# Kernel tuning notes

Hardware: AMD Instinct MI355X
Metric: run time of the kernel (lower is better)

The kernel has to match this reference:

```python
import jax, jax.numpy as jnp
import numpy as np

N_CUST = 500000
N_FUND = 50000
N_EDGE = 4000000
D_CUST = 101
D_FUND = 1
HID = 64


def setup_inputs() -> dict:
    key = jax.random.key(0)
    ks = jax.random.split(key, 16)
    s = lambda fan_in: 1.0 / np.sqrt(fan_in)
    return {
        "x_customer": jax.random.normal(ks[0], (N_CUST, D_CUST), jnp.float32),
        "x_fund": jax.random.normal(ks[1], (N_FUND, D_FUND), jnp.float32),
        "src_fund": jax.random.randint(ks[2], (N_EDGE,), 0, N_FUND, jnp.int64),
        "dst_customer": jax.random.randint(ks[3], (N_EDGE,), 0, N_CUST, jnp.int64),
        # per-node-type input projections
        "W_cust": jax.random.uniform(ks[4], (D_CUST, HID), jnp.float32, -s(D_CUST), s(D_CUST)),
        "b_cust": jax.random.uniform(ks[5], (HID,), jnp.float32, -s(D_CUST), s(D_CUST)),
        "W_fund": jax.random.uniform(ks[6], (D_FUND, HID), jnp.float32, -s(D_FUND), s(D_FUND)),
        "b_fund": jax.random.uniform(ks[7], (HID,), jnp.float32, -s(D_FUND), s(D_FUND)),
        # SAGEConv fund->customer: lin_l (neighbor aggr, bias) + lin_r (self, no bias)
        "W_l": jax.random.uniform(ks[8], (HID, HID), jnp.float32, -s(HID), s(HID)),
        "b_l": jax.random.uniform(ks[9], (HID,), jnp.float32, -s(HID), s(HID)),
        "W_r": jax.random.uniform(ks[10], (HID, HID), jnp.float32, -s(HID), s(HID)),
        # output head
        "W_out": jax.random.uniform(ks[11], (HID, 2), jnp.float32, -s(HID), s(HID)),
        "b_out": jax.random.uniform(ks[12], (2,), jnp.float32, -s(HID), s(HID)),
    }


def reference(x_customer, x_fund, src_fund, dst_customer,
              W_cust, b_cust, W_fund, b_fund, W_l, b_l, W_r, W_out, b_out):
    # per-node-type linear + relu
    h_c = jax.nn.relu(x_customer @ W_cust + b_cust)  # [N_CUST, HID]
    h_f = jax.nn.relu(x_fund @ W_fund + b_fund)      # [N_FUND, HID]

    # SAGEConv (fund -> customer): gather src fund features per edge,
    # mean-aggregate by destination customer (scatter-sum / count)
    msgs = h_f[src_fund]  # [N_EDGE, HID]
    summed = jax.ops.segment_sum(msgs, dst_customer, num_segments=N_CUST)
    cnt = jax.ops.segment_sum(jnp.ones((msgs.shape[0],), msgs.dtype),
                              dst_customer, num_segments=N_CUST)
    mean = summed / jnp.maximum(cnt, 1.0)[:, None]

    out_c = mean @ W_l + b_l + h_c @ W_r  # SAGE: lin_l(aggr) + lin_r(self)
    return out_c @ W_out + b_out          # [N_CUST, 2]
```

## Files before the change

kernel.cpp:

```cpp
#include <hip/hip_runtime.h>
#include <stdint.h>

#define N_CUST 500000
#define N_FUND 50000
#define N_EDGE 4000000
#define D_CUST 101
#define HID 64

#define NB   512
#define EPB  ((N_EDGE + NB - 1) / NB)
#define CB   512
#define NBKT ((N_CUST + CB - 1) / CB)
#define CAP  8192
#define TPB  32

typedef float  float4u __attribute__((ext_vector_type(4), aligned(4)));
using frag_ab = __attribute__((ext_vector_type(8))) short;
using frag_cd = __attribute__((ext_vector_type(4))) float;

struct __align__(16) Accum { float g0, g1, cnt, pad; };

__device__ __forceinline__ short f2bf(float f) {
    unsigned u = __float_as_uint(f);
    u += 0x7fffu + ((u >> 16) & 1u);
    return (short)(u >> 16);
}

__global__ __launch_bounds__(256) void k_gf(
    const float* __restrict__ x_fund,
    const float* __restrict__ W_fund,
    const float* __restrict__ b_fund,
    const float* __restrict__ W_l,
    const float* __restrict__ W_out,
    float2* __restrict__ gf)
{
    __shared__ float sAf[128];
    __shared__ float sWf[64];
    __shared__ float sBf[64];
    int t = threadIdx.x;
    if (t < 128) {
        int h = t >> 1, j = t & 1;
        float s = 0.f;
        for (int k = 0; k < 64; ++k)
            s = fmaf(W_l[h * 64 + k], W_out[k * 2 + j], s);
        sAf[t] = s;
    } else if (t < 192) {
        sWf[t - 128] = W_fund[t - 128];
    } else {
        sBf[t - 192] = b_fund[t - 192];
    }
    __syncthreads();

    int f = blockIdx.x * 256 + t;
    if (f >= N_FUND) return;
    float xf = x_fund[f];
    float g0 = 0.f, g1 = 0.f;
    #pragma unroll
    for (int h = 0; h < 64; ++h) {
        float hf = fmaxf(fmaf(xf, sWf[h], sBf[h]), 0.f);
        g0 = fmaf(hf, sAf[2 * h + 0], g0);
        g1 = fmaf(hf, sAf[2 * h + 1], g1);
    }
    gf[f] = make_float2(g0, g1);
}

__global__ __launch_bounds__(256) void k_reorder(
    const int* __restrict__ src, const int* __restrict__ dst,
    unsigned* __restrict__ gcur, unsigned* __restrict__ recs)
{
    __shared__ unsigned hist[NBKT];
    __shared__ unsigned localOff[NBKT];
    __shared__ unsigned cur[NBKT];
    __shared__ unsigned baseG[NBKT];
    __shared__ unsigned ldsRec[EPB];
    __shared__ unsigned short ldsBkt[EPB];

    int t = threadIdx.x, b = blockIdx.x;
    int e0 = b * EPB, e1 = min(e0 + EPB, N_EDGE);
    int cntE = e1 - e0;

    for (int k = t; k < NBKT; k += 256) hist[k] = 0;
    __syncthreads();
    for (int e = e0 + t; e < e1; e += 256)
        atomicAdd(&hist[((unsigned)dst[e]) >> 9], 1u);
    __syncthreads();

    if (t < 64) {
        unsigned v[16], pre[16], run = 0;
        #pragma unroll
        for (int j = 0; j < 16; ++j) {
            int idx = t * 16 + j;
            v[j] = (idx < NBKT) ? hist[idx] : 0u;
            pre[j] = run; run += v[j];
        }
        unsigned sc = run;
        #pragma unroll
        for (int d = 1; d < 64; d <<= 1) {
            unsigned n = __shfl_up(sc, d, 64);
            if (t >= d) sc += n;
        }
        unsigned lane_excl = sc - run;
        #pragma unroll
        for (int j = 0; j < 16; ++j) {
            int idx = t * 16 + j;
            if (idx < NBKT) {
                localOff[idx] = lane_excl + pre[j];
                cur[idx]      = lane_excl + pre[j];
            }
        }
    }
    __syncthreads();

    for (int k = t; k < NBKT; k += 256) {
        unsigned h = hist[k];
        baseG[k] = h ? ((unsigned)k * CAP + atomicAdd(&gcur[k], h)) : 0u;
    }

    for (int e = e0 + t; e < e1; e += 256) {
        unsigned d = (unsigned)dst[e];
        unsigned s = (unsigned)src[e];
        unsigned k = d >> 9;
        unsigned p = atomicAdd(&cur[k], 1u);
        ldsRec[p] = s | ((d & 511u) << 16);
        ldsBkt[p] = (unsigned short)k;
    }
    __syncthreads();

    for (int i = t; i < cntE; i += 256) {
        unsigned k = ldsBkt[i];
        unsigned g = baseG[k] + (i - localOff[k]);
        recs[g] = ldsRec[i];
    }
}

__global__ __launch_bounds__(256) void k_bucket(
    const unsigned* __restrict__ recs, const unsigned* __restrict__ gcur,
    const float2* __restrict__ gf,
    const float* __restrict__ x, const float* __restrict__ Wc,
    const float* __restrict__ bc,
    const float* __restrict__ W_r, const float* __restrict__ W_out,
    const float* __restrict__ b_l, const float* __restrict__ b_out,
    float2* __restrict__ out)
{
    __shared__ float s0[CB], s1[CB], scn[CB];
    __shared__ float sBt[128];
    __shared__ float sc2[2];
    __shared__ float zb[4][16 * 68];

    int t = threadIdx.x, k = blockIdx.x;

    if (t < 128) {
        int h = t >> 1, j = t & 1;
        float s = 0.f;
        for (int kk = 0; kk < 64; ++kk)
            s = fmaf(W_r[h * 64 + kk], W_out[kk * 2 + j], s);
        sBt[t] = s;
    } else if (t < 130) {
        int j = t - 128;
        float s = b_out[j];
        for (int kk = 0; kk < 64; ++kk)
            s = fmaf(b_l[kk], W_out[kk * 2 + j], s);
        sc2[j] = s;
    }
    for (int c = t; c < CB; c += 256) { s0[c] = 0.f; s1[c] = 0.f; scn[c] = 0.f; }
    __syncthreads();

    unsigned r0 = (unsigned)k * CAP, r1 = r0 + gcur[k];
    for (unsigned i = r0 + t; i < r1; i += 256) {
        unsigned r = recs[i];
        float2 g = gf[r & 0xFFFFu];
        unsigned dl = r >> 16;
        atomicAdd(&s0[dl], g.x);
        atomicAdd(&s1[dl], g.y);
        atomicAdd(&scn[dl], 1.f);
    }

    int w = t >> 6, lane = t & 63;
    int c = lane & 15, q = lane >> 4;
    float* z = zb[w];
    frag_ab bfrag[4][4];
    for (int nt = 0; nt < 4; ++nt)
        for (int kc = 0; kc < 4; ++kc) {
            frag_ab f;
            for (int j = 0; j < 8; ++j) {
                int kk = kc * 32 + q * 8 + j;
                int h = nt * 16 + c;
                f[j] = (kk < D_CUST) ? f2bf(Wc[kk * HID + h]) : (short)0;
            }
            bfrag[nt][kc] = f;
        }
    float bcv[4];
    #pragma unroll
    for (int nt = 0; nt < 4; ++nt) bcv[nt] = bc[nt * 16 + c];
    __syncthreads();

    float c20 = sc2[0], c21 = sc2[1];
    int cust0 = k * CB;
    int n_tiles = min(TPB, (N_CUST - cust0) >> 4);

    for (int tl = w; tl < n_tiles; tl += 4) {
        int lrow = tl * 16 + c;
        int row = cust0 + lrow;
        const float* xr = x + (size_t)row * D_CUST;
        frag_ab af[4];
        #pragma unroll
        for (int kc = 0; kc < 3; ++kc) {
            float4u lo = *(const float4u*)(xr + kc * 32 + q * 8);
            float4u hi = *(const float4u*)(xr + kc * 32 + q * 8 + 4);
            frag_ab f;
            f[0]=f2bf(lo[0]); f[1]=f2bf(lo[1]); f[2]=f2bf(lo[2]); f[3]=f2bf(lo[3]);
            f[4]=f2bf(hi[0]); f[5]=f2bf(hi[1]); f[6]=f2bf(hi[2]); f[7]=f2bf(hi[3]);
            af[kc] = f;
        }
        {
            frag_ab f = {0,0,0,0,0,0,0,0};
            if (q == 0) {
                float4u lo = *(const float4u*)(xr + 96);
                f[0]=f2bf(lo[0]); f[1]=f2bf(lo[1]); f[2]=f2bf(lo[2]); f[3]=f2bf(lo[3]);
                f[4]=f2bf(xr[100]);
            }
            af[3] = f;
        }
        frag_cd acc[4];
        #pragma unroll
        for (int nt = 0; nt < 4; ++nt)
            acc[nt] = (frag_cd){bcv[nt], bcv[nt], bcv[nt], bcv[nt]};
        #pragma unroll
        for (int kc = 0; kc < 4; ++kc)
            #pragma unroll
            for (int nt = 0; nt < 4; ++nt)
                acc[nt] = __builtin_amdgcn_mfma_f32_16x16x32_bf16(
                    af[kc], bfrag[nt][kc], acc[nt], 0, 0, 0);

        #pragma unroll
        for (int nt = 0; nt < 4; ++nt)
            #pragma unroll
            for (int i = 0; i < 4; ++i)
                z[(q * 4 + i) * 68 + nt * 16 + c] = fmaxf(acc[nt][i], 0.f);

        float p0 = 0.f, p1 = 0.f;
        #pragma unroll
        for (int j4 = 0; j4 < 4; ++j4) {
            float4u zv = *(const float4u*)(z + c * 68 + q * 16 + j4 * 4);
            float4u b0 = *(const float4u*)(sBt + q * 32 + j4 * 8);
            float4u b1 = *(const float4u*)(sBt + q * 32 + j4 * 8 + 4);
            p0 = fmaf(zv[0], b0[0], p0); p1 = fmaf(zv[0], b0[1], p1);
            p0 = fmaf(zv[1], b0[2], p0); p1 = fmaf(zv[1], b0[3], p1);
            p0 = fmaf(zv[2], b1[0], p0); p1 = fmaf(zv[2], b1[1], p1);
            p0 = fmaf(zv[3], b1[2], p0); p1 = fmaf(zv[3], b1[3], p1);
        }
        p0 += __shfl_xor(p0, 16, 64); p0 += __shfl_xor(p0, 32, 64);
        p1 += __shfl_xor(p1, 16, 64); p1 += __shfl_xor(p1, 32, 64);
        if (q == 0) {
            float inv = 1.0f / fmaxf(scn[lrow], 1.0f);
            out[cust0 + lrow] = make_float2(fmaf(s0[lrow], inv, p0 + c20),
                                            fmaf(s1[lrow], inv, p1 + c21));
        }
    }
}

__global__ __launch_bounds__(256) void k_prep_fb(
    const float* __restrict__ W_r, const float* __restrict__ W_out,
    const float* __restrict__ b_l, const float* __restrict__ b_out,
    float* __restrict__ Bt, float* __restrict__ c2)
{
    int t = threadIdx.x;
    if (t < 128) {
        int h = t >> 1, j = t & 1;
        float s = 0.f;
        for (int k = 0; k < 64; ++k)
            s = fmaf(W_r[h * 64 + k], W_out[k * 2 + j], s);
        Bt[t] = s;
    } else if (t < 130) {
        int j = t - 128;
        float s = b_out[j];
        for (int k = 0; k < 64; ++k)
            s = fmaf(b_l[k], W_out[k * 2 + j], s);
        c2[j] = s;
    }
}

__global__ __launch_bounds__(256) void k_scatter_direct(
    const int* __restrict__ src, const int* __restrict__ dst,
    const float2* __restrict__ gf, Accum* __restrict__ A)
{
    int stride = gridDim.x * 256;
    for (int e = blockIdx.x * 256 + threadIdx.x; e < N_EDGE; e += stride) {
        int s = src[e], d = dst[e];
        float2 g = gf[s];
        unsafeAtomicAdd(&A[d].g0, g.x);
        unsafeAtomicAdd(&A[d].g1, g.y);
        unsafeAtomicAdd(&A[d].cnt, 1.0f);
    }
}

__global__ __launch_bounds__(256) void k_cust_fb(
    const float* __restrict__ x, const float* __restrict__ Wc,
    const float* __restrict__ bc, const float* __restrict__ Bt,
    const float* __restrict__ c2, const Accum* __restrict__ A,
    float2* __restrict__ out)
{
    __shared__ float zb[4][16 * 68];
    __shared__ float sBt[128];
    int tid = threadIdx.x;
    int w = tid >> 6, lane = tid & 63;
    int c = lane & 15, q = lane >> 4;
    float* z = zb[w];
    if (tid < 128) sBt[tid] = Bt[tid];

    frag_ab bfrag[4][4];
    for (int nt = 0; nt < 4; ++nt)
        for (int kc = 0; kc < 4; ++kc) {
            frag_ab f;
            for (int j = 0; j < 8; ++j) {
                int k = kc * 32 + q * 8 + j;
                f[j] = (k < D_CUST) ? f2bf(Wc[k * HID + nt * 16 + c]) : (short)0;
            }
            bfrag[nt][kc] = f;
        }
    float bcv[4];
    #pragma unroll
    for (int nt = 0; nt < 4; ++nt) bcv[nt] = bc[nt * 16 + c];
    float c20 = c2[0], c21 = c2[1];
    __syncthreads();

    int wglob = blockIdx.x * 4 + w;
    int wstride = gridDim.x * 4;
    for (int t = wglob; t < N_CUST / 16; t += wstride) {
        int row = t * 16 + c;
        const float* xr = x + (size_t)row * D_CUST;
        frag_ab af[4];
        #pragma unroll
        for (int kc = 0; kc < 3; ++kc) {
            float4u lo = *(const float4u*)(xr + kc * 32 + q * 8);
            float4u hi = *(const float4u*)(xr + kc * 32 + q * 8 + 4);
            frag_ab f;
            f[0]=f2bf(lo[0]); f[1]=f2bf(lo[1]); f[2]=f2bf(lo[2]); f[3]=f2bf(lo[3]);
            f[4]=f2bf(hi[0]); f[5]=f2bf(hi[1]); f[6]=f2bf(hi[2]); f[7]=f2bf(hi[3]);
            af[kc] = f;
        }
        {
            frag_ab f = {0,0,0,0,0,0,0,0};
            if (q == 0) {
                float4u lo = *(const float4u*)(xr + 96);
                f[0]=f2bf(lo[0]); f[1]=f2bf(lo[1]); f[2]=f2bf(lo[2]); f[3]=f2bf(lo[3]);
                f[4]=f2bf(xr[100]);
            }
            af[3] = f;
        }
        frag_cd acc[4];
        #pragma unroll
        for (int nt = 0; nt < 4; ++nt)
            acc[nt] = (frag_cd){bcv[nt], bcv[nt], bcv[nt], bcv[nt]};
        #pragma unroll
        for (int kc = 0; kc < 4; ++kc)
            #pragma unroll
            for (int nt = 0; nt < 4; ++nt)
                acc[nt] = __builtin_amdgcn_mfma_f32_16x16x32_bf16(
                    af[kc], bfrag[nt][kc], acc[nt], 0, 0, 0);
        #pragma unroll
        for (int nt = 0; nt < 4; ++nt)
            #pragma unroll
            for (int i = 0; i < 4; ++i)
                z[(q * 4 + i) * 68 + nt * 16 + c] = fmaxf(acc[nt][i], 0.f);
        float p0 = 0.f, p1 = 0.f;
        #pragma unroll
        for (int j4 = 0; j4 < 4; ++j4) {
            float4u zv = *(const float4u*)(z + c * 68 + q * 16 + j4 * 4);
            float4u b0 = *(const float4u*)(sBt + q * 32 + j4 * 8);
            float4u b1 = *(const float4u*)(sBt + q * 32 + j4 * 8 + 4);
            p0 = fmaf(zv[0], b0[0], p0); p1 = fmaf(zv[0], b0[1], p1);
            p0 = fmaf(zv[1], b0[2], p0); p1 = fmaf(zv[1], b0[3], p1);
            p0 = fmaf(zv[2], b1[0], p0); p1 = fmaf(zv[2], b1[1], p1);
            p0 = fmaf(zv[3], b1[2], p0); p1 = fmaf(zv[3], b1[3], p1);
        }
        p0 += __shfl_xor(p0, 16, 64); p0 += __shfl_xor(p0, 32, 64);
        p1 += __shfl_xor(p1, 16, 64); p1 += __shfl_xor(p1, 32, 64);
        if (q == 0) {
            Accum a = A[t * 16 + c];
            float inv = 1.0f / fmaxf(a.cnt, 1.0f);
            out[t * 16 + c] = make_float2(fmaf(a.g0, inv, p0 + c20),
                                          fmaf(a.g1, inv, p1 + c21));
        }
    }
}

extern "C" void kernel_launch(void* const* d_in, const int* in_sizes, int n_in,
                              void* d_out, int out_size, void* d_ws, size_t ws_size,
                              hipStream_t stream) {
    const float* x_customer = (const float*)d_in[0];
    const float* x_fund     = (const float*)d_in[1];
    const int*   src_fund   = (const int*)d_in[2];
    const int*   dst_cust   = (const int*)d_in[3];
    const float* W_cust     = (const float*)d_in[4];
    const float* b_cust     = (const float*)d_in[5];
    const float* W_fund     = (const float*)d_in[6];
    const float* b_fund     = (const float*)d_in[7];
    const float* W_l        = (const float*)d_in[8];
    const float* b_l        = (const float*)d_in[9];
    const float* W_r        = (const float*)d_in[10];
    const float* W_out      = (const float*)d_in[11];
    const float* b_out      = (const float*)d_in[12];

    char* ws = (char*)d_ws;
    const size_t NEED = 404096ull + (size_t)NBKT * CAP * 4ull;

    if (ws_size >= NEED) {
        float2*   gf   = (float2*)  (ws);
        unsigned* gcur = (unsigned*)(ws + 400000);
        unsigned* recs = (unsigned*)(ws + 404096);

        hipMemsetAsync(gcur, 0, NBKT * sizeof(unsigned), stream);
        k_gf<<<(N_FUND + 255) / 256, 256, 0, stream>>>(
            x_fund, W_fund, b_fund, W_l, W_out, gf);
        k_reorder<<<NB, 256, 0, stream>>>(src_fund, dst_cust, gcur, recs);
        k_bucket<<<NBKT, 256, 0, stream>>>(
            recs, gcur, gf, x_customer, W_cust, b_cust,
            W_r, W_out, b_l, b_out, (float2*)d_out);
    } else {
        Accum*  A  = (Accum*) (ws);
        float2* gf = (float2*)(ws + 8000000);
        float*  Bt = (float*) (ws + 8400000);
        float*  c2 = (float*) (ws + 8400512);

        hipMemsetAsync(A, 0, sizeof(Accum) * (size_t)N_CUST, stream);
        k_prep_fb<<<1, 256, 0, stream>>>(W_r, W_out, b_l, b_out, Bt, c2);
        k_gf<<<(N_FUND + 255) / 256, 256, 0, stream>>>(
            x_fund, W_fund, b_fund, W_l, W_out, gf);
        k_scatter_direct<<<2048, 256, 0, stream>>>(src_fund, dst_cust, gf, A);
        k_cust_fb<<<1024, 256, 0, stream>>>(
            x_customer, W_cust, b_cust, Bt, c2, A, (float2*)d_out);
    }
}
```

Before: 425.6 us.

## Fuse edge scatter and customer MFMA into one interleaved kernel

Drops the bucketed reorder path (histogram, LDS sort, bucket kernel). It now runs one fused kernel whose work items interleave chunks of direct global-atomic edge scatter with 64-row customer MFMA tiles, so the latency-bound atomics overlap with the bandwidth-bound x_customer streaming. Zeroing of the accumulator, the folded W_r·W_out weights and the pre-swizzled bf16 W_cust fragments move into the first kernel, which removes the memset and the per-block fragment rebuild. A small final kernel applies the mean division. The cost is contended global float atomics on 16-byte records and an extra read-modify-write pass over the output.

```diff
diff --git a/kernel.cpp b/kernel.cpp
--- a/kernel.cpp
+++ b/kernel.cpp
@@ -7,14 +7,14 @@
 #define D_CUST 101
 #define HID 64
 
-#define NB   512
-#define EPB  ((N_EDGE + NB - 1) / NB)
-#define CB   512
-#define NBKT ((N_CUST + CB - 1) / CB)
-#define CAP  8192
-#define TPB  32
-
-typedef float  float4u __attribute__((ext_vector_type(4), aligned(4)));
+#define GF_GRID 512
+#define FU_GRID 2048
+#define EPI     4096
+#define SITEMS  ((N_EDGE + EPI - 1) / EPI)
+#define GITEMS  ((N_CUST + 63) / 64)
+#define NW      (SITEMS * 9)
+
+typedef float float4u __attribute__((ext_vector_type(4), aligned(4)));
 using frag_ab = __attribute__((ext_vector_type(8))) short;
 using frag_cd = __attribute__((ext_vector_type(4))) float;
 
@@ -31,13 +31,28 @@
     const float* __restrict__ W_fund,
     const float* __restrict__ b_fund,
     const float* __restrict__ W_l,
+    const float* __restrict__ W_r,
     const float* __restrict__ W_out,
-    float2* __restrict__ gf)
+    const float* __restrict__ Wc,
+    const float* __restrict__ b_l,
+    const float* __restrict__ b_out,
+    float2* __restrict__ gf,
+    frag_ab* __restrict__ wcb,
+    float* __restrict__ Bt,
+    float* __restrict__ c2,
+    float4* __restrict__ Az)
 {
     __shared__ float sAf[128];
     __shared__ float sWf[64];
     __shared__ float sBf[64];
     int t = threadIdx.x;
+
+    {
+        float4 z4 = make_float4(0.f, 0.f, 0.f, 0.f);
+        for (int i = blockIdx.x * 256 + t; i < N_CUST; i += GF_GRID * 256)
+            Az[i] = z4;
+    }
+
     if (t < 128) {
         int h = t >> 1, j = t & 1;
         float s = 0.f;
@@ -52,337 +67,163 @@
     __syncthreads();
 
     int f = blockIdx.x * 256 + t;
-    if (f >= N_FUND) return;
-    float xf = x_fund[f];
-    float g0 = 0.f, g1 = 0.f;
-    #pragma unroll
-    for (int h = 0; h < 64; ++h) {
-        float hf = fmaxf(fmaf(xf, sWf[h], sBf[h]), 0.f);
-        g0 = fmaf(hf, sAf[2 * h + 0], g0);
-        g1 = fmaf(hf, sAf[2 * h + 1], g1);
-    }
-    gf[f] = make_float2(g0, g1);
-}
-
-__global__ __launch_bounds__(256) void k_reorder(
+    if (f < N_FUND) {
+        float xf = x_fund[f];
+        float g0 = 0.f, g1 = 0.f;
+        #pragma unroll
+        for (int h = 0; h < 64; ++h) {
+            float hf = fmaxf(fmaf(xf, sWf[h], sBf[h]), 0.f);
+            g0 = fmaf(hf, sAf[2 * h + 0], g0);
+            g1 = fmaf(hf, sAf[2 * h + 1], g1);
+        }
+        gf[f] = make_float2(g0, g1);
+    }
+
+    if (blockIdx.x == 0) {
+        if (t < 128) {
+            int h = t >> 1, j = t & 1;
+            float s = 0.f;
+            for (int k = 0; k < 64; ++k)
+                s = fmaf(W_r[h * 64 + k], W_out[k * 2 + j], s);
+            Bt[t] = s;
+        } else if (t < 130) {
+            int j = t - 128;
+            float s = b_out[j];
+            for (int k = 0; k < 64; ++k)
+                s = fmaf(b_l[k], W_out[k * 2 + j], s);
+            c2[j] = s;
+        }
+        for (int sidx = t; sidx < 1024; sidx += 256) {
+            int fidx = sidx >> 6, l = sidx & 63;
+            int c = l & 15, q = l >> 4;
+            int nt = fidx >> 2, kc = fidx & 3;
+            frag_ab fr;
+            #pragma unroll
+            for (int j = 0; j < 8; ++j) {
+                int kk = kc * 32 + q * 8 + j;
+                int h  = nt * 16 + c;
+                fr[j] = (kk < D_CUST) ? f2bf(Wc[kk * HID + h]) : (short)0;
+            }
+            wcb[sidx] = fr;
+        }
+    }
+}
+
+__global__ __launch_bounds__(256) void k_fused(
     const int* __restrict__ src, const int* __restrict__ dst,
-    unsigned* __restrict__ gcur, unsigned* __restrict__ recs)
+    const float2* __restrict__ gf, Accum* __restrict__ A,
+    const float* __restrict__ x, const float* __restrict__ bc,
+    const frag_ab* __restrict__ wcb, const float* __restrict__ Bt,
+    const float* __restrict__ c2, float2* __restrict__ out)
 {
-    __shared__ unsigned hist[NBKT];
-    __shared__ unsigned localOff[NBKT];
-    __shared__ unsigned cur[NBKT];
-    __shared__ unsigned baseG[NBKT];
-    __shared__ unsigned ldsRec[EPB];
-    __shared__ unsigned short ldsBkt[EPB];
-
-    int t = threadIdx.x, b = blockIdx.x;
-    int e0 = b * EPB, e1 = min(e0 + EPB, N_EDGE);
-    int cntE = e1 - e0;
-
-    for (int k = t; k < NBKT; k += 256) hist[k] = 0;
-    __syncthreads();
-    for (int e = e0 + t; e < e1; e += 256)
-        atomicAdd(&hist[((unsigned)dst[e]) >> 9], 1u);
-    __syncthreads();
-
-    if (t < 64) {
-        unsigned v[16], pre[16], run = 0;
-        #pragma unroll
-        for (int j = 0; j < 16; ++j) {
-            int idx = t * 16 + j;
-            v[j] = (idx < NBKT) ? hist[idx] : 0u;
-            pre[j] = run; run += v[j];
-        }
-        unsigned sc = run;
-        #pragma unroll
-        for (int d = 1; d < 64; d <<= 1) {
-            unsigned n = __shfl_up(sc, d, 64);
-            if (t >= d) sc += n;
-        }
-        unsigned lane_excl = sc - run;
-        #pragma unroll
-        for (int j = 0; j < 16; ++j) {
-            int idx = t * 16 + j;
-            if (idx < NBKT) {
-                localOff[idx] = lane_excl + pre[j];
-                cur[idx]      = lane_excl + pre[j];
-            }
-        }
-    }
-    __syncthreads();
-
-    for (int k = t; k < NBKT; k += 256) {
-        unsigned h = hist[k];
-        baseG[k] = h ? ((unsigned)k * CAP + atomicAdd(&gcur[k], h)) : 0u;
-    }
-
-    for (int e = e0 + t; e < e1; e += 256) {
-        unsigned d = (unsigned)dst[e];
-        unsigned s = (unsigned)src[e];
-        unsigned k = d >> 9;
-        unsigned p = atomicAdd(&cur[k], 1u);
-        ldsRec[p] = s | ((d & 511u) << 16);
-        ldsBkt[p] = (unsigned short)k;
-    }
-    __syncthreads();
-
-    for (int i = t; i < cntE; i += 256) {
-        unsigned k = ldsBkt[i];
-        unsigned g = baseG[k] + (i - localOff[k]);
-        recs[g] = ldsRec[i];
-    }
-}
-
-__global__ __launch_bounds__(256) void k_bucket(
-    const unsigned* __restrict__ recs, const unsigned* __restrict__ gcur,
-    const float2* __restrict__ gf,
-    const float* __restrict__ x, const float* __restrict__ Wc,
-    const float* __restrict__ bc,
-    const float* __restrict__ W_r, const float* __restrict__ W_out,
-    const float* __restrict__ b_l, const float* __restrict__ b_out,
-    float2* __restrict__ out)
-{
-    __shared__ float s0[CB], s1[CB], scn[CB];
     __shared__ float sBt[128];
-    __shared__ float sc2[2];
     __shared__ float zb[4][16 * 68];
 
-    int t = threadIdx.x, k = blockIdx.x;
-
-    if (t < 128) {
-        int h = t >> 1, j = t & 1;
-        float s = 0.f;
-        for (int kk = 0; kk < 64; ++kk)
-            s = fmaf(W_r[h * 64 + kk], W_out[kk * 2 + j], s);
-        sBt[t] = s;
-    } else if (t < 130) {
-        int j = t - 128;
-        float s = b_out[j];
-        for (int kk = 0; kk < 64; ++kk)
-            s = fmaf(b_l[kk], W_out[kk * 2 + j], s);
-        sc2[j] = s;
-    }
-    for (int c = t; c < CB; c += 256) { s0[c] = 0.f; s1[c] = 0.f; scn[c] = 0.f; }
-    __syncthreads();
-
-    unsigned r0 = (unsigned)k * CAP, r1 = r0 + gcur[k];
-    for (unsigned i = r0 + t; i < r1; i += 256) {
-        unsigned r = recs[i];
-        float2 g = gf[r & 0xFFFFu];
-        unsigned dl = r >> 16;
-        atomicAdd(&s0[dl], g.x);
-        atomicAdd(&s1[dl], g.y);
-        atomicAdd(&scn[dl], 1.f);
-    }
-
+    int t = threadIdx.x;
     int w = t >> 6, lane = t & 63;
     int c = lane & 15, q = lane >> 4;
     float* z = zb[w];
-    frag_ab bfrag[4][4];
-    for (int nt = 0; nt < 4; ++nt)
-        for (int kc = 0; kc < 4; ++kc) {
-            frag_ab f;
-            for (int j = 0; j < 8; ++j) {
-                int kk = kc * 32 + q * 8 + j;
-                int h = nt * 16 + c;
-                f[j] = (kk < D_CUST) ? f2bf(Wc[kk * HID + h]) : (short)0;
-            }
-            bfrag[nt][kc] = f;
-        }
-    float bcv[4];
+
+    if (t < 128) sBt[t] = Bt[t];
+    frag_ab bfrag[16];
     #pragma unroll
-    for (int nt = 0; nt < 4; ++nt) bcv[nt] = bc[nt * 16 + c];
-    __syncthreads();
-
-    float c20 = sc2[0], c21 = sc2[1];
-    int cust0 = k * CB;
-    int n_tiles = min(TPB, (N_CUST - cust0) >> 4);
-
-    for (int tl = w; tl < n_tiles; tl += 4) {
-        int lrow = tl * 16 + c;
-        int row = cust0 + lrow;
-        const float* xr = x + (size_t)row * D_CUST;
-        frag_ab af[4];
-        #pragma unroll
-        for (int kc = 0; kc < 3; ++kc) {
-            float4u lo = *(const float4u*)(xr + kc * 32 + q * 8);
-            float4u hi = *(const float4u*)(xr + kc * 32 + q * 8 + 4);
-            frag_ab f;
-            f[0]=f2bf(lo[0]); f[1]=f2bf(lo[1]); f[2]=f2bf(lo[2]); f[3]=f2bf(lo[3]);
-            f[4]=f2bf(hi[0]); f[5]=f2bf(hi[1]); f[6]=f2bf(hi[2]); f[7]=f2bf(hi[3]);
-            af[kc] = f;
-        }
-        {
-            frag_ab f = {0,0,0,0,0,0,0,0};
-            if (q == 0) {
-                float4u lo = *(const float4u*)(xr + 96);
-                f[0]=f2bf(lo[0]); f[1]=f2bf(lo[1]); f[2]=f2bf(lo[2]); f[3]=f2bf(lo[3]);
-                f[4]=f2bf(xr[100]);
-            }
-            af[3] = f;
-        }
-        frag_cd acc[4];
-        #pragma unroll
-        for (int nt = 0; nt < 4; ++nt)
-            acc[nt] = (frag_cd){bcv[nt], bcv[nt], bcv[nt], bcv[nt]};
-        #pragma unroll
-        for (int kc = 0; kc < 4; ++kc)
-            #pragma unroll
-            for (int nt = 0; nt < 4; ++nt)
-                acc[nt] = __builtin_amdgcn_mfma_f32_16x16x32_bf16(
-                    af[kc], bfrag[nt][kc], acc[nt], 0, 0, 0);
-
-        #pragma unroll
-        for (int nt = 0; nt < 4; ++nt)
-            #pragma unroll
-            for (int i = 0; i < 4; ++i)
-                z[(q * 4 + i) * 68 + nt * 16 + c] = fmaxf(acc[nt][i], 0.f);
-
-        float p0 = 0.f, p1 = 0.f;
-        #pragma unroll
-        for (int j4 = 0; j4 < 4; ++j4) {
-            float4u zv = *(const float4u*)(z + c * 68 + q * 16 + j4 * 4);
-            float4u b0 = *(const float4u*)(sBt + q * 32 + j4 * 8);
-            float4u b1 = *(const float4u*)(sBt + q * 32 + j4 * 8 + 4);
-            p0 = fmaf(zv[0], b0[0], p0); p1 = fmaf(zv[0], b0[1], p1);
-            p0 = fmaf(zv[1], b0[2], p0); p1 = fmaf(zv[1], b0[3], p1);
-            p0 = fmaf(zv[2], b1[0], p0); p1 = fmaf(zv[2], b1[1], p1);
-            p0 = fmaf(zv[3], b1[2], p0); p1 = fmaf(zv[3], b1[3], p1);
-        }
-        p0 += __shfl_xor(p0, 16, 64); p0 += __shfl_xor(p0, 32, 64);
-        p1 += __shfl_xor(p1, 16, 64); p1 += __shfl_xor(p1, 32, 64);
-        if (q == 0) {
-            float inv = 1.0f / fmaxf(scn[lrow], 1.0f);
-            out[cust0 + lrow] = make_float2(fmaf(s0[lrow], inv, p0 + c20),
-                                            fmaf(s1[lrow], inv, p1 + c21));
-        }
-    }
-}
-
-__global__ __launch_bounds__(256) void k_prep_fb(
-    const float* __restrict__ W_r, const float* __restrict__ W_out,
-    const float* __restrict__ b_l, const float* __restrict__ b_out,
-    float* __restrict__ Bt, float* __restrict__ c2)
-{
-    int t = threadIdx.x;
-    if (t < 128) {
-        int h = t >> 1, j = t & 1;
-        float s = 0.f;
-        for (int k = 0; k < 64; ++k)
-            s = fmaf(W_r[h * 64 + k], W_out[k * 2 + j], s);
-        Bt[t] = s;
-    } else if (t < 130) {
-        int j = t - 128;
-        float s = b_out[j];
-        for (int k = 0; k < 64; ++k)
-            s = fmaf(b_l[k], W_out[k * 2 + j], s);
-        c2[j] = s;
-    }
-}
-
-__global__ __launch_bounds__(256) void k_scatter_direct(
-    const int* __restrict__ src, const int* __restrict__ dst,
-    const float2* __restrict__ gf, Accum* __restrict__ A)
-{
-    int stride = gridDim.x * 256;
-    for (int e = blockIdx.x * 256 + threadIdx.x; e < N_EDGE; e += stride) {
-        int s = src[e], d = dst[e];
-        float2 g = gf[s];
-        unsafeAtomicAdd(&A[d].g0, g.x);
-        unsafeAtomicAdd(&A[d].g1, g.y);
-        unsafeAtomicAdd(&A[d].cnt, 1.0f);
-    }
-}
-
-__global__ __launch_bounds__(256) void k_cust_fb(
-    const float* __restrict__ x, const float* __restrict__ Wc,
-    const float* __restrict__ bc, const float* __restrict__ Bt,
-    const float* __restrict__ c2, const Accum* __restrict__ A,
-    float2* __restrict__ out)
-{
-    __shared__ float zb[4][16 * 68];
-    __shared__ float sBt[128];
-    int tid = threadIdx.x;
-    int w = tid >> 6, lane = tid & 63;
-    int c = lane & 15, q = lane >> 4;
-    float* z = zb[w];
-    if (tid < 128) sBt[tid] = Bt[tid];
-
-    frag_ab bfrag[4][4];
-    for (int nt = 0; nt < 4; ++nt)
-        for (int kc = 0; kc < 4; ++kc) {
-            frag_ab f;
-            for (int j = 0; j < 8; ++j) {
-                int k = kc * 32 + q * 8 + j;
-                f[j] = (k < D_CUST) ? f2bf(Wc[k * HID + nt * 16 + c]) : (short)0;
-            }
-            bfrag[nt][kc] = f;
-        }
+    for (int f = 0; f < 16; ++f) bfrag[f] = wcb[f * 64 + lane];
     float bcv[4];
     #pragma unroll
     for (int nt = 0; nt < 4; ++nt) bcv[nt] = bc[nt * 16 + c];
     float c20 = c2[0], c21 = c2[1];
     __syncthreads();
 
-    int wglob = blockIdx.x * 4 + w;
-    int wstride = gridDim.x * 4;
-    for (int t = wglob; t < N_CUST / 16; t += wstride) {
-        int row = t * 16 + c;
-        const float* xr = x + (size_t)row * D_CUST;
-        frag_ab af[4];
-        #pragma unroll
-        for (int kc = 0; kc < 3; ++kc) {
-            float4u lo = *(const float4u*)(xr + kc * 32 + q * 8);
-            float4u hi = *(const float4u*)(xr + kc * 32 + q * 8 + 4);
-            frag_ab f;
-            f[0]=f2bf(lo[0]); f[1]=f2bf(lo[1]); f[2]=f2bf(lo[2]); f[3]=f2bf(lo[3]);
-            f[4]=f2bf(hi[0]); f[5]=f2bf(hi[1]); f[6]=f2bf(hi[2]); f[7]=f2bf(hi[3]);
-            af[kc] = f;
-        }
-        {
-            frag_ab f = {0,0,0,0,0,0,0,0};
-            if (q == 0) {
-                float4u lo = *(const float4u*)(xr + 96);
+    for (int wi = blockIdx.x; wi < NW; wi += gridDim.x) {
+        int d9 = wi / 9;
+        if (wi - d9 * 9 == 8) {
+            int e1 = min(d9 * EPI + EPI, N_EDGE);
+            for (int e = d9 * EPI + t * 4; e < e1; e += 1024) {
+                int4 s4 = *(const int4*)(src + e);
+                int4 d4 = *(const int4*)(dst + e);
+                float2 g0 = gf[s4.x], g1 = gf[s4.y];
+                float2 g2 = gf[s4.z], g3 = gf[s4.w];
+                Accum* a0 = A + d4.x; Accum* a1 = A + d4.y;
+                Accum* a2 = A + d4.z; Accum* a3 = A + d4.w;
+                unsafeAtomicAdd(&a0->g0, g0.x); unsafeAtomicAdd(&a0->g1, g0.y);
+                unsafeAtomicAdd(&a0->cnt, 1.f);
+                unsafeAtomicAdd(&a1->g0, g1.x); unsafeAtomicAdd(&a1->g1, g1.y);
+                unsafeAtomicAdd(&a1->cnt, 1.f);
+                unsafeAtomicAdd(&a2->g0, g2.x); unsafeAtomicAdd(&a2->g1, g2.y);
+                unsafeAtomicAdd(&a2->cnt, 1.f);
+                unsafeAtomicAdd(&a3->g0, g3.x); unsafeAtomicAdd(&a3->g1, g3.y);
+                unsafeAtomicAdd(&a3->cnt, 1.f);
+            }
+        } else {
+            int g = wi - d9;
+            if (g >= GITEMS) continue;
+            int row0 = g * 64 + w * 16;
+            if (row0 >= N_CUST) continue;
+            const float* xr = x + (size_t)(row0 + c) * D_CUST;
+            frag_ab af[4];
+            #pragma unroll
+            for (int kc = 0; kc < 3; ++kc) {
+                float4u lo = *(const float4u*)(xr + kc * 32 + q * 8);
+                float4u hi = *(const float4u*)(xr + kc * 32 + q * 8 + 4);
+                frag_ab f;
                 f[0]=f2bf(lo[0]); f[1]=f2bf(lo[1]); f[2]=f2bf(lo[2]); f[3]=f2bf(lo[3]);
-                f[4]=f2bf(xr[100]);
-            }
-            af[3] = f;
-        }
-        frag_cd acc[4];
-        #pragma unroll
-        for (int nt = 0; nt < 4; ++nt)
-            acc[nt] = (frag_cd){bcv[nt], bcv[nt], bcv[nt], bcv[nt]};
-        #pragma unroll
-        for (int kc = 0; kc < 4; ++kc)
+                f[4]=f2bf(hi[0]); f[5]=f2bf(hi[1]); f[6]=f2bf(hi[2]); f[7]=f2bf(hi[3]);
+                af[kc] = f;
+            }
+            {
+                frag_ab f = {0,0,0,0,0,0,0,0};
+                if (q == 0) {
+                    float4u lo = *(const float4u*)(xr + 96);
+                    f[0]=f2bf(lo[0]); f[1]=f2bf(lo[1]); f[2]=f2bf(lo[2]); f[3]=f2bf(lo[3]);
+                    f[4]=f2bf(xr[100]);
+                }
+                af[3] = f;
+            }
+            frag_cd acc[4];
             #pragma unroll
             for (int nt = 0; nt < 4; ++nt)
-                acc[nt] = __builtin_amdgcn_mfma_f32_16x16x32_bf16(
-                    af[kc], bfrag[nt][kc], acc[nt], 0, 0, 0);
-        #pragma unroll
-        for (int nt = 0; nt < 4; ++nt)
-            #pragma unroll
-            for (int i = 0; i < 4; ++i)
-                z[(q * 4 + i) * 68 + nt * 16 + c] = fmaxf(acc[nt][i], 0.f);
-        float p0 = 0.f, p1 = 0.f;
-        #pragma unroll
-        for (int j4 = 0; j4 < 4; ++j4) {
-            float4u zv = *(const float4u*)(z + c * 68 + q * 16 + j4 * 4);
-            float4u b0 = *(const float4u*)(sBt + q * 32 + j4 * 8);
-            float4u b1 = *(const float4u*)(sBt + q * 32 + j4 * 8 + 4);
-            p0 = fmaf(zv[0], b0[0], p0); p1 = fmaf(zv[0], b0[1], p1);
-            p0 = fmaf(zv[1], b0[2], p0); p1 = fmaf(zv[1], b0[3], p1);
-            p0 = fmaf(zv[2], b1[0], p0); p1 = fmaf(zv[2], b1[1], p1);
-            p0 = fmaf(zv[3], b1[2], p0); p1 = fmaf(zv[3], b1[3], p1);
-        }
-        p0 += __shfl_xor(p0, 16, 64); p0 += __shfl_xor(p0, 32, 64);
-        p1 += __shfl_xor(p1, 16, 64); p1 += __shfl_xor(p1, 32, 64);
-        if (q == 0) {
-            Accum a = A[t * 16 + c];
-            float inv = 1.0f / fmaxf(a.cnt, 1.0f);
-            out[t * 16 + c] = make_float2(fmaf(a.g0, inv, p0 + c20),
-                                          fmaf(a.g1, inv, p1 + c21));
-        }
-    }
+                acc[nt] = (frag_cd){bcv[nt], bcv[nt], bcv[nt], bcv[nt]};
+            #pragma unroll
+            for (int kc = 0; kc < 4; ++kc)
+                #pragma unroll
+                for (int nt = 0; nt < 4; ++nt)
+                    acc[nt] = __builtin_amdgcn_mfma_f32_16x16x32_bf16(
+                        af[kc], bfrag[nt * 4 + kc], acc[nt], 0, 0, 0);
+
+            #pragma unroll
+            for (int nt = 0; nt < 4; ++nt)
+                #pragma unroll
+                for (int i = 0; i < 4; ++i)
+                    z[(q * 4 + i) * 68 + nt * 16 + c] = fmaxf(acc[nt][i], 0.f);
+
+            float p0 = 0.f, p1 = 0.f;
+            #pragma unroll
+            for (int j4 = 0; j4 < 4; ++j4) {
+                float4u zv = *(const float4u*)(z + c * 68 + q * 16 + j4 * 4);
+                float4u b0 = *(const float4u*)(sBt + q * 32 + j4 * 8);
+                float4u b1 = *(const float4u*)(sBt + q * 32 + j4 * 8 + 4);
+                p0 = fmaf(zv[0], b0[0], p0); p1 = fmaf(zv[0], b0[1], p1);
+                p0 = fmaf(zv[1], b0[2], p0); p1 = fmaf(zv[1], b0[3], p1);
+                p0 = fmaf(zv[2], b1[0], p0); p1 = fmaf(zv[2], b1[1], p1);
+                p0 = fmaf(zv[3], b1[2], p0); p1 = fmaf(zv[3], b1[3], p1);
+            }
+            p0 += __shfl_xor(p0, 16, 64); p0 += __shfl_xor(p0, 32, 64);
+            p1 += __shfl_xor(p1, 16, 64); p1 += __shfl_xor(p1, 32, 64);
+            if (q == 0)
+                out[row0 + c] = make_float2(p0 + c20, p1 + c21);
+        }
+    }
+}
+
+__global__ __launch_bounds__(256) void k_final(
+    const Accum* __restrict__ A, float2* __restrict__ out)
+{
+    int cidx = blockIdx.x * 256 + threadIdx.x;
+    if (cidx >= N_CUST) return;
+    Accum a = A[cidx];
+    float inv = 1.0f / fmaxf(a.cnt, 1.0f);
+    float2 o = out[cidx];
+    out[cidx] = make_float2(fmaf(a.g0, inv, o.x), fmaf(a.g1, inv, o.y));
 }
 
 extern "C" void kernel_launch(void* const* d_in, const int* in_sizes, int n_in,
@@ -403,32 +244,17 @@
     const float* b_out      = (const float*)d_in[12];
 
     char* ws = (char*)d_ws;
-    const size_t NEED = 404096ull + (size_t)NBKT * CAP * 4ull;
-
-    if (ws_size >= NEED) {
-        float2*   gf   = (float2*)  (ws);
-        unsigned* gcur = (unsigned*)(ws + 400000);
-        unsigned* recs = (unsigned*)(ws + 404096);
-
-        hipMemsetAsync(gcur, 0, NBKT * sizeof(unsigned), stream);
-        k_gf<<<(N_FUND + 255) / 256, 256, 0, stream>>>(
-            x_fund, W_fund, b_fund, W_l, W_out, gf);
-        k_reorder<<<NB, 256, 0, stream>>>(src_fund, dst_cust, gcur, recs);
-        k_bucket<<<NBKT, 256, 0, stream>>>(
-            recs, gcur, gf, x_customer, W_cust, b_cust,
-            W_r, W_out, b_l, b_out, (float2*)d_out);
-    } else {
-        Accum*  A  = (Accum*) (ws);
-        float2* gf = (float2*)(ws + 8000000);
-        float*  Bt = (float*) (ws + 8400000);
-        float*  c2 = (float*) (ws + 8400512);
-
-        hipMemsetAsync(A, 0, sizeof(Accum) * (size_t)N_CUST, stream);
-        k_prep_fb<<<1, 256, 0, stream>>>(W_r, W_out, b_l, b_out, Bt, c2);
-        k_gf<<<(N_FUND + 255) / 256, 256, 0, stream>>>(
-            x_fund, W_fund, b_fund, W_l, W_out, gf);
-        k_scatter_direct<<<2048, 256, 0, stream>>>(src_fund, dst_cust, gf, A);
-        k_cust_fb<<<1024, 256, 0, stream>>>(
-            x_customer, W_cust, b_cust, Bt, c2, A, (float2*)d_out);
-    }
-}
+    Accum*   A   = (Accum*)  (ws);
+    float2*  gf  = (float2*) (ws + 8000000);
+    frag_ab* wcb = (frag_ab*)(ws + 8400000);
+    float*   Bt  = (float*)  (ws + 8416384);
+    float*   c2  = (float*)  (ws + 8416896);
+
+    k_gf<<<GF_GRID, 256, 0, stream>>>(
+        x_fund, W_fund, b_fund, W_l, W_r, W_out, W_cust, b_l, b_out,
+        gf, wcb, Bt, c2, (float4*)A);
+    k_fused<<<FU_GRID, 256, 0, stream>>>(
+        src_fund, dst_cust, gf, A, x_customer, b_cust, wcb, Bt, c2,
+        (float2*)d_out);
+    k_final<<<(N_CUST + 255) / 256, 256, 0, stream>>>(A, (float2*)d_out);
+}
```

Measured after the change: 875.9 us. 106% more time.
